# Kernel tuning notes

Measured on AMD Instinct MI355X. Metric: run time of the kernel, lower is better.

The kernel has to match this reference:

```python
import jax, jax.numpy as jnp
import numpy as np

NUM_CLASSES = 100
QUEUE_SIZE = 256
FEATURE_DIM = 1024
BATCH = 4096
EPS = 1e-12  # torch F.normalize eps


def _l2norm(x):
    n = jnp.linalg.norm(x, axis=-1, keepdims=True)
    return x / jnp.maximum(n, EPS)


def setup_inputs() -> dict:
    key = jax.random.key(0)
    k1, k2, k3, k4 = jax.random.split(key, 4)
    embeddings = jax.random.normal(k1, (BATCH, FEATURE_DIM), dtype=jnp.float32)
    labels = jax.random.randint(k2, (BATCH,), 0, NUM_CLASSES, dtype=jnp.int64)
    # buffer initialized as randn then L2-normalized (as in __init__)
    queue = _l2norm(jax.random.normal(k3, (NUM_CLASSES, QUEUE_SIZE, FEATURE_DIM), dtype=jnp.float32))
    queue_ptr = jax.random.randint(k4, (NUM_CLASSES,), 0, QUEUE_SIZE, dtype=jnp.int64)
    return {"embeddings": embeddings, "labels": labels, "queue": queue, "queue_ptr": queue_ptr}


def reference(embeddings, labels, queue, queue_ptr):
    # MemoryBank.update with tail_classes=None: store_idx == label.
    # Serial FIFO semantics: the k-th occurrence of class c in the batch is
    # written at slot (queue_ptr[c] + k) % queue_size.
    queue_size = queue.shape[1]
    emb = _l2norm(embeddings.astype(jnp.float32))  # (B, d)
    # rank[b] = number of earlier batch elements with the same label
    same = labels[:, None] == labels[None, :]           # (B, B)
    rank = jnp.sum(jnp.tril(same, k=-1), axis=1)        # (B,)
    slots = (queue_ptr[labels] + rank) % queue_size      # (B,)
    new_queue = queue.at[labels, slots].set(emb)
    return new_queue
```

## Files before the change

### kernel.cpp

```cpp
#include <hip/hip_runtime.h>

#define NUM_CLASSES 100
#define QUEUE_SIZE  256
#define FEATURE_DIM 1024
#define BATCH       4096
#define TOTAL_ROWS  (NUM_CLASSES * QUEUE_SIZE)
#define EPS         1e-12f

typedef float f32x4 __attribute__((ext_vector_type(4)));

__global__ __launch_bounds__(256) void compute_slots_kernel(
    const int* __restrict__ labels,
    const int* __restrict__ queue_ptr,
    int* __restrict__ inv)
{
    __shared__ int hist[NUM_CLASSES];
    __shared__ int s_lab[256];

    const int tid = threadIdx.x;
    const int chunk_start = blockIdx.x * 256;

    for (int i = tid; i < NUM_CLASSES; i += 256) hist[i] = 0;
    __syncthreads();

    for (int j = tid; j < chunk_start; j += 256) {
        atomicAdd(&hist[labels[j]], 1);
    }
    s_lab[tid] = labels[chunk_start + tid];
    __syncthreads();

    const int lab = s_lab[tid];
    int rank = hist[lab];
    for (int j = 0; j < tid; ++j) {
        rank += (s_lab[j] == lab) ? 1 : 0;
    }
    const int slot = (queue_ptr[lab] + rank) & (QUEUE_SIZE - 1);
    const int row  = lab * QUEUE_SIZE + slot;
    atomicMax(&inv[row], chunk_start + tid);
}

__global__ __launch_bounds__(256) void fused_write_kernel(
    const float* __restrict__ queue,
    const float* __restrict__ emb,
    const int* __restrict__ inv,
    float* __restrict__ out)
{
    const int tid  = threadIdx.x;
    const int lane = tid & 63;
    const int wave = tid >> 6;
    const int row  = blockIdx.x * 4 + wave;
    const long base = (long)row * FEATURE_DIM;

    const int b = inv[row];
    f32x4* dst = reinterpret_cast<f32x4*>(out + base);

    if (b < 0) {
        const f32x4* src = reinterpret_cast<const f32x4*>(queue + base);
        f32x4 v0 = src[lane];
        f32x4 v1 = src[lane + 64];
        f32x4 v2 = src[lane + 128];
        f32x4 v3 = src[lane + 192];
        __builtin_nontemporal_store(v0, &dst[lane]);
        __builtin_nontemporal_store(v1, &dst[lane + 64]);
        __builtin_nontemporal_store(v2, &dst[lane + 128]);
        __builtin_nontemporal_store(v3, &dst[lane + 192]);
    } else {
        const f32x4* src = reinterpret_cast<const f32x4*>(emb + (long)b * FEATURE_DIM);
        f32x4 v0 = src[lane];
        f32x4 v1 = src[lane + 64];
        f32x4 v2 = src[lane + 128];
        f32x4 v3 = src[lane + 192];

        float ss = v0.x*v0.x + v0.y*v0.y + v0.z*v0.z + v0.w*v0.w
                 + v1.x*v1.x + v1.y*v1.y + v1.z*v1.z + v1.w*v1.w
                 + v2.x*v2.x + v2.y*v2.y + v2.z*v2.z + v2.w*v2.w
                 + v3.x*v3.x + v3.y*v3.y + v3.z*v3.z + v3.w*v3.w;
        #pragma unroll
        for (int off = 32; off; off >>= 1) {
            ss += __shfl_xor(ss, off, 64);
        }
        const float s = 1.0f / fmaxf(sqrtf(ss), EPS);

        __builtin_nontemporal_store(v0 * s, &dst[lane]);
        __builtin_nontemporal_store(v1 * s, &dst[lane + 64]);
        __builtin_nontemporal_store(v2 * s, &dst[lane + 128]);
        __builtin_nontemporal_store(v3 * s, &dst[lane + 192]);
    }
}

extern "C" void kernel_launch(void* const* d_in, const int* in_sizes, int n_in,
                              void* d_out, int out_size, void* d_ws, size_t ws_size,
                              hipStream_t stream)
{
    const float* embeddings = (const float*)d_in[0];
    const int*   labels     = (const int*)d_in[1];
    const float* queue      = (const float*)d_in[2];
    const int*   queue_ptr  = (const int*)d_in[3];

    float* out = (float*)d_out;
    int*   inv = (int*)d_ws;

    (void)hipMemsetAsync(inv, 0xFF, TOTAL_ROWS * sizeof(int), stream);

    compute_slots_kernel<<<BATCH / 256, 256, 0, stream>>>(labels, queue_ptr, inv);

    fused_write_kernel<<<TOTAL_ROWS / 4, 256, 0, stream>>>(
        queue, embeddings, inv, out);
}
```

Baseline: 48.76 us.

## Compute slot inverse per class with ballot compaction, drop memset and atomics

Replaces the per-chunk histogram-plus-atomicMax slot kernel with one block per class that compacts the batch indices of that class in order using wave ballots, then directly assigns each queue slot the last writer. This removes the memset launch and the atomic scatter, and writes the inverse map densely. It also switches the main copy kernel from nontemporal stores to plain stores, which changes cache behavior for the large output write. Each class block scans all labels serially in one wave, which adds latency to the small kernel.

```diff
diff --git a/kernel.cpp b/kernel.cpp
--- a/kernel.cpp
+++ b/kernel.cpp
@@ -9,34 +9,43 @@
 
 typedef float f32x4 __attribute__((ext_vector_type(4)));
 
-__global__ __launch_bounds__(256) void compute_slots_kernel(
+__global__ __launch_bounds__(256) void slots_direct_kernel(
     const int* __restrict__ labels,
     const int* __restrict__ queue_ptr,
     int* __restrict__ inv)
 {
-    __shared__ int hist[NUM_CLASSES];
-    __shared__ int s_lab[256];
+    __shared__ int occ[BATCH];
+    __shared__ int s_cnt;
 
-    const int tid = threadIdx.x;
-    const int chunk_start = blockIdx.x * 256;
+    const int c    = blockIdx.x;
+    const int tid  = threadIdx.x;
+    const int lane = tid & 63;
 
-    for (int i = tid; i < NUM_CLASSES; i += 256) hist[i] = 0;
+    if (tid < 64) {
+        int base = 0;
+        const unsigned long long lt = (1ULL << lane) - 1ULL;
+        #pragma unroll 4
+        for (int i = 0; i < BATCH / 64; ++i) {
+            const int b = i * 64 + lane;
+            const bool m = (labels[b] == c);
+            const unsigned long long mask = __ballot(m);
+            if (m) occ[base + __popcll(mask & lt)] = b;
+            base += __popcll(mask);
+        }
+        if (lane == 0) s_cnt = base;
+    }
     __syncthreads();
 
-    for (int j = tid; j < chunk_start; j += 256) {
-        atomicAdd(&hist[labels[j]], 1);
+    const int cnt = s_cnt;
+    const int p   = queue_ptr[c] & (QUEUE_SIZE - 1);
+    const int s   = tid;
+    const int k0  = (s - p) & (QUEUE_SIZE - 1);
+    int b = -1;
+    if (k0 < cnt) {
+        const int k = k0 + (((cnt - 1 - k0) >> 8) << 8);
+        b = occ[k];
     }
-    s_lab[tid] = labels[chunk_start + tid];
-    __syncthreads();
-
-    const int lab = s_lab[tid];
-    int rank = hist[lab];
-    for (int j = 0; j < tid; ++j) {
-        rank += (s_lab[j] == lab) ? 1 : 0;
-    }
-    const int slot = (queue_ptr[lab] + rank) & (QUEUE_SIZE - 1);
-    const int row  = lab * QUEUE_SIZE + slot;
-    atomicMax(&inv[row], chunk_start + tid);
+    inv[c * QUEUE_SIZE + s] = b;
 }
 
 __global__ __launch_bounds__(256) void fused_write_kernel(
@@ -60,10 +69,10 @@
         f32x4 v1 = src[lane + 64];
         f32x4 v2 = src[lane + 128];
         f32x4 v3 = src[lane + 192];
-        __builtin_nontemporal_store(v0, &dst[lane]);
-        __builtin_nontemporal_store(v1, &dst[lane + 64]);
-        __builtin_nontemporal_store(v2, &dst[lane + 128]);
-        __builtin_nontemporal_store(v3, &dst[lane + 192]);
+        dst[lane]       = v0;
+        dst[lane + 64]  = v1;
+        dst[lane + 128] = v2;
+        dst[lane + 192] = v3;
     } else {
         const f32x4* src = reinterpret_cast<const f32x4*>(emb + (long)b * FEATURE_DIM);
         f32x4 v0 = src[lane];
@@ -79,12 +88,12 @@
         for (int off = 32; off; off >>= 1) {
             ss += __shfl_xor(ss, off, 64);
         }
-        const float s = 1.0f / fmaxf(sqrtf(ss), EPS);
+        const float sc = 1.0f / fmaxf(sqrtf(ss), EPS);
 
-        __builtin_nontemporal_store(v0 * s, &dst[lane]);
-        __builtin_nontemporal_store(v1 * s, &dst[lane + 64]);
-        __builtin_nontemporal_store(v2 * s, &dst[lane + 128]);
-        __builtin_nontemporal_store(v3 * s, &dst[lane + 192]);
+        dst[lane]       = v0 * sc;
+        dst[lane + 64]  = v1 * sc;
+        dst[lane + 128] = v2 * sc;
+        dst[lane + 192] = v3 * sc;
     }
 }
 
@@ -100,9 +109,7 @@
     float* out = (float*)d_out;
     int*   inv = (int*)d_ws;
 
-    (void)hipMemsetAsync(inv, 0xFF, TOTAL_ROWS * sizeof(int), stream);
-
-    compute_slots_kernel<<<BATCH / 256, 256, 0, stream>>>(labels, queue_ptr, inv);
+    slots_direct_kernel<<<NUM_CLASSES, 256, 0, stream>>>(labels, queue_ptr, inv);
 
     fused_write_kernel<<<TOTAL_ROWS / 4, 256, 0, stream>>>(
         queue, embeddings, inv, out);
```

Result: slower. 54.23 us (+11.2%).
